# Optimization experiments

Hardware: AMD Instinct MI355X
Metric: run time of the kernel (lower is better)

## Reference

```python
import jax, jax.numpy as jnp
import numpy as np

N_HEADS = 16
D_EMBED = 1024
HEAD_DIM = D_EMBED // N_HEADS


def setup_inputs() -> dict:
    key = jax.random.key(0)
    ks = jax.random.split(key, 9)
    s = 1.0 / np.sqrt(D_EMBED)
    def lin(kw, kb):
        W = jax.random.uniform(kw, (D_EMBED, D_EMBED), jnp.float32, -s, s)
        b = jax.random.uniform(kb, (D_EMBED,), jnp.float32, -s, s)
        return W, b
    q_w, q_b = lin(ks[0], ks[1])
    k_w, k_b = lin(ks[2], ks[3])
    v_w, v_b = lin(ks[4], ks[5])
    o_w, o_b = lin(ks[6], ks[7])
    x = jax.random.normal(ks[8], (4, 2048, D_EMBED), jnp.float32)
    return {"x": x, "q_w": q_w, "q_b": q_b, "k_w": k_w, "k_b": k_b,
            "v_w": v_w, "v_b": v_b, "o_w": o_w, "o_b": o_b}


def reference(x, q_w, q_b, k_w, k_b, v_w, v_b, o_w, o_b):
    B, S, _ = x.shape
    # projections; W stored as [in, out] so y = x @ W + b (matches nn.Linear math)
    def split_heads(y):
        return y.reshape(B, S, N_HEADS, HEAD_DIM).transpose(0, 2, 1, 3)  # [B,H,S,D]
    q = split_heads(x @ q_w + q_b)
    k = split_heads(x @ k_w + k_b)
    v = split_heads(x @ v_w + v_b)
    scale = 1.0 / np.sqrt(HEAD_DIM).astype(np.float32)
    scores = jnp.einsum('bhqd,bhkd->bhqk', q, k) * scale  # [B,H,S,S]
    weights = jax.nn.softmax(scores, axis=-1)
    attn = jnp.einsum('bhqk,bhkd->bhqd', weights, v)  # [B,H,S,D]
    attn = attn.transpose(0, 2, 1, 3).reshape(B, S, D_EMBED)
    return attn @ o_w + o_b
```

## Files before the change

kernel.cpp:

```cpp
#include <hip/hip_runtime.h>
#include <hip/hip_bf16.h>
#include <math.h>

typedef __attribute__((ext_vector_type(8))) short bf16x8;
typedef __attribute__((ext_vector_type(4))) float f32x4;

#define D_EMBED 1024
#define SEQ 2048
#define NH 16
#define HD 64
#define QSCALE 0.1803368801111204f

__device__ __forceinline__ short f2bf(float f) {
    union { float f; unsigned u; } v; v.f = f;
    return (short)((v.u + 0x7FFFu + ((v.u >> 16) & 1u)) >> 16);
}

__device__ __forceinline__ unsigned pk_bf16(float a, float b) {
#if __has_builtin(__builtin_amdgcn_cvt_pk_bf16_f32)
    typedef __attribute__((ext_vector_type(2))) __bf16 vbf2;
    union { vbf2 v; unsigned u; } c;
    c.v = __builtin_amdgcn_cvt_pk_bf16_f32(a, b);
    return c.u;
#else
    return (unsigned)(unsigned short)f2bf(a) | ((unsigned)(unsigned short)f2bf(b) << 16);
#endif
}

__device__ __forceinline__ float exp2f_(float x) {
#if __has_builtin(__builtin_amdgcn_exp2f)
    return __builtin_amdgcn_exp2f(x);
#else
    return __expf(x * 0.6931471805599453f);
#endif
}

typedef __attribute__((address_space(1))) const void gvoid_t;
typedef __attribute__((address_space(3))) void lvoid_t;
__device__ __forceinline__ void glds16(const void* g, void* l) {
    __builtin_amdgcn_global_load_lds((gvoid_t*)g, (lvoid_t*)l, 16, 0, 0);
}

__global__ __launch_bounds__(256) void prep_kernel(
    const float* __restrict__ x,
    const float* __restrict__ w0, const float* __restrict__ w1,
    const float* __restrict__ w2, const float* __restrict__ w3,
    short* __restrict__ wt, short* __restrict__ xb)
{
    __shared__ float tile[64][65];
    const int bid = blockIdx.x;
    if (bid < 1024) {
        const int z = bid >> 8, rem = bid & 255;
        const float* W = (z == 0) ? w0 : (z == 1) ? w1 : (z == 2) ? w2 : w3;
        short* out = wt + (size_t)z * D_EMBED * D_EMBED;
        int k0 = (rem & 15) * 64, n0 = (rem >> 4) * 64;
        #pragma unroll
        for (int i = 0; i < 16; i++) {
            int idx = threadIdx.x + i * 256; int r = idx >> 6, c = idx & 63;
            tile[r][c] = W[(size_t)(k0 + r) * D_EMBED + n0 + c];
        }
        __syncthreads();
        #pragma unroll
        for (int i = 0; i < 16; i++) {
            int idx = threadIdx.x + i * 256; int r = idx >> 6, c = idx & 63;
            out[(size_t)(n0 + r) * D_EMBED + k0 + c] = f2bf(tile[c][r]);
        }
    } else {
        size_t i = ((size_t)(bid - 1024) * 256 + threadIdx.x) * 8;
        float4 f0 = *(const float4*)(x + i);
        float4 f1 = *(const float4*)(x + i + 4);
        uint4 o;
        o.x = pk_bf16(f0.x, f0.y); o.y = pk_bf16(f0.z, f0.w);
        o.z = pk_bf16(f1.x, f1.y); o.w = pk_bf16(f1.z, f1.w);
        *(uint4*)(xb + i) = o;
    }
}

__global__ __launch_bounds__(256) void gemm_qkv_kernel(
    const short* __restrict__ xb, const short* __restrict__ wt,
    const float* __restrict__ qb, const float* __restrict__ kb, const float* __restrict__ vb,
    short* __restrict__ qo, short* __restrict__ ko, short* __restrict__ vto)
{
    __shared__ __attribute__((aligned(16))) union ShQKV {
        struct { short As[128][32]; short Bs[128][32]; } ab;
        short Es[64][136];
    } sh;
    const int tid = threadIdx.x;
    const int lane = tid & 63, wv = tid >> 6;
    const int l16 = lane & 15, quad = lane >> 4;
    const int wm = (wv & 1) * 64, wn = (wv >> 1) * 64;
    const int m0 = blockIdx.y * 128, n0 = blockIdx.x * 128;

    const short* aptr0 = xb + (size_t)(m0 + (tid >> 2)) * D_EMBED + (tid & 3) * 8;
    const short* aptr1 = aptr0 + (size_t)64 * D_EMBED;
    const short* bptr0 = wt + (size_t)(n0 + (tid >> 2)) * D_EMBED + (tid & 3) * 8;
    const short* bptr1 = bptr0 + (size_t)64 * D_EMBED;
    char* aldsb = (char*)&sh.ab.As[0][0] + wv * 1024;
    char* bldsb = (char*)&sh.ab.Bs[0][0] + wv * 1024;

    f32x4 acc[4][4];
    #pragma unroll
    for (int a = 0; a < 4; a++)
        #pragma unroll
        for (int b = 0; b < 4; b++) acc[a][b] = (f32x4){0.f, 0.f, 0.f, 0.f};

    for (int k0 = 0; k0 < D_EMBED; k0 += 32) {
        __syncthreads();
        glds16(aptr0 + k0, aldsb);
        glds16(aptr1 + k0, aldsb + 4096);
        glds16(bptr0 + k0, bldsb);
        glds16(bptr1 + k0, bldsb + 4096);
        __syncthreads();
        bf16x8 af[4], bfr[4];
        #pragma unroll
        for (int mi = 0; mi < 4; mi++) af[mi]  = *(const bf16x8*)&sh.ab.As[wm + mi * 16 + l16][quad * 8];
        #pragma unroll
        for (int ni = 0; ni < 4; ni++) bfr[ni] = *(const bf16x8*)&sh.ab.Bs[wn + ni * 16 + l16][quad * 8];
        #pragma unroll
        for (int mi = 0; mi < 4; mi++)
            #pragma unroll
            for (int ni = 0; ni < 4; ni++)
                acc[mi][ni] = __builtin_amdgcn_mfma_f32_16x16x32_bf16(af[mi], bfr[ni], acc[mi][ni], 0, 0, 0);
    }

    const int zz = n0 >> 10;
    if (zz == 2) {
        const int b = m0 >> 11, st0 = m0 & 2047;
        const int hbase = (n0 & 1023) >> 6;
        #pragma unroll
        for (int h2 = 0; h2 < 2; h2++) {
            __syncthreads();
            if ((wv >> 1) == h2) {
                #pragma unroll
                for (int mi = 0; mi < 4; mi++) {
                    int sbase = (wv & 1) * 64 + mi * 16 + quad * 4;
                    #pragma unroll
                    for (int ni = 0; ni < 4; ni++) {
                        int d = ni * 16 + l16;
                        float bv = vb[(n0 & 1023) + h2 * 64 + d];
                        uint2 pw;
                        pw.x = pk_bf16(acc[mi][ni][0] + bv, acc[mi][ni][1] + bv);
                        pw.y = pk_bf16(acc[mi][ni][2] + bv, acc[mi][ni][3] + bv);
                        *(uint2*)&sh.Es[d][sbase] = pw;
                    }
                }
            }
            __syncthreads();
            const int h = hbase + h2;
            #pragma unroll
            for (int j = 0; j < 4; j++) {
                int d = j * 16 + (tid >> 4);
                int sc = (tid & 15) * 8;
                bf16x8 vv = *(const bf16x8*)&sh.Es[d][sc];
                *(bf16x8*)(vto + ((size_t)(b * NH + h) * HD + d) * SEQ + st0 + sc) = vv;
            }
        }
    } else {
        const int ncol0 = (n0 & 1023) + wn;
        const float* bias = (zz == 0) ? qb : kb;
        #pragma unroll
        for (int mi = 0; mi < 4; mi++)
            #pragma unroll
            for (int ni = 0; ni < 4; ni++)
                #pragma unroll
                for (int rg = 0; rg < 4; rg++) {
                    int row = m0 + wm + mi * 16 + quad * 4 + rg;
                    int col = ncol0 + ni * 16 + l16;
                    float v = acc[mi][ni][rg] + bias[col];
                    int b = row >> 11, s = row & 2047, h = col >> 6, d = col & 63;
                    if (zz == 0) qo[(((size_t)(b * NH + h)) * SEQ + s) * HD + d] = f2bf(v * QSCALE);
                    else         ko[(((size_t)(b * NH + h)) * SEQ + s) * HD + d] = f2bf(v);
                }
    }
}

__global__ __launch_bounds__(256) void flash_kernel(
    const short* __restrict__ Q, const short* __restrict__ K,
    const short* __restrict__ Vt, short* __restrict__ attn)
{
    __shared__ __attribute__((aligned(16))) short Vs[64][64];
    __shared__ __attribute__((aligned(16))) short Ps[4][64][72];
    const int bh = blockIdx.y, qt = blockIdx.x;
    const int tid = threadIdx.x, lane = tid & 63, wv = tid >> 6;
    const int l16 = lane & 15, quad = lane >> 4;
    const int sw = l16 & 7;

    bf16x8 qf[4][2];
    #pragma unroll
    for (int g = 0; g < 4; g++) {
        const short* qp = Q + ((size_t)bh * SEQ + qt * 256 + wv * 64 + g * 16 + l16) * HD;
        qf[g][0] = *(const bf16x8*)(qp + quad * 8);
        qf[g][1] = *(const bf16x8*)(qp + 32 + quad * 8);
    }

    const int sr = tid >> 3;
    const int scg = (tid & 7) ^ (sr & 7);
    const short* vp0 = Vt + ((size_t)bh * HD + sr) * SEQ + scg * 8;
    char* vldsb = (char*)&Vs[0][0] + wv * 1024;

    const short* kb0 = K + ((size_t)bh * SEQ + l16) * HD + quad * 8;

    float lsum[4] = {0.f, 0.f, 0.f, 0.f};
    f32x4 oacc[4][4];
    #pragma unroll
    for (int g = 0; g < 4; g++)
        #pragma unroll
        for (int di = 0; di < 4; di++) oacc[g][di] = (f32x4){0.f, 0.f, 0.f, 0.f};

    for (int kt = 0; kt < SEQ; kt += 64) {
        __syncthreads();
        glds16(vp0 + kt, vldsb);
        glds16(vp0 + (size_t)32 * SEQ + kt, vldsb + 4096);

        bf16x8 kf[4][2];
        #pragma unroll
        for (int ni = 0; ni < 4; ni++) {
            const short* kp = kb0 + (size_t)(kt + ni * 16) * HD;
            kf[ni][0] = *(const bf16x8*)kp;
            kf[ni][1] = *(const bf16x8*)(kp + 32);
        }

        #pragma unroll
        for (int g = 0; g < 4; g++) {
            f32x4 sacc[4];
            #pragma unroll
            for (int ni = 0; ni < 4; ni++) {
                sacc[ni] = (f32x4){0.f, 0.f, 0.f, 0.f};
                sacc[ni] = __builtin_amdgcn_mfma_f32_16x16x32_bf16(kf[ni][0], qf[g][0], sacc[ni], 0, 0, 0);
                sacc[ni] = __builtin_amdgcn_mfma_f32_16x16x32_bf16(kf[ni][1], qf[g][1], sacc[ni], 0, 0, 0);
            }
            short* prow = &Ps[wv][g * 16 + l16][0];
            float ps = 0.f;
            #pragma unroll
            for (int ni = 0; ni < 4; ni++) {
                float p0 = exp2f_(sacc[ni][0]);
                float p1 = exp2f_(sacc[ni][1]);
                float p2 = exp2f_(sacc[ni][2]);
                float p3 = exp2f_(sacc[ni][3]);
                ps += (p0 + p1) + (p2 + p3);
                uint2 pw; pw.x = pk_bf16(p0, p1); pw.y = pk_bf16(p2, p3);
                *(uint2*)(prow + ni * 16 + quad * 4) = pw;
            }
            lsum[g] += ps;
        }

        __syncthreads();

        bf16x8 vf[4][2];
        #pragma unroll
        for (int di = 0; di < 4; di++) {
            vf[di][0] = *(const bf16x8*)&Vs[di * 16 + l16][((quad    ) ^ sw) * 8];
            vf[di][1] = *(const bf16x8*)&Vs[di * 16 + l16][((quad + 4) ^ sw) * 8];
        }
        #pragma unroll
        for (int g = 0; g < 4; g++) {
            const short* prow = &Ps[wv][g * 16 + l16][0];
            bf16x8 pf0 = *(const bf16x8*)(prow + quad * 8);
            bf16x8 pf1 = *(const bf16x8*)(prow + 32 + quad * 8);
            #pragma unroll
            for (int di = 0; di < 4; di++) {
                oacc[g][di] = __builtin_amdgcn_mfma_f32_16x16x32_bf16(pf0, vf[di][0], oacc[g][di], 0, 0, 0);
                oacc[g][di] = __builtin_amdgcn_mfma_f32_16x16x32_bf16(pf1, vf[di][1], oacc[g][di], 0, 0, 0);
            }
        }
    }

    const int b = bh >> 4, h = bh & 15;
    #pragma unroll
    for (int g = 0; g < 4; g++) {
        float l = lsum[g];
        l += __shfl_xor(l, 16);
        l += __shfl_xor(l, 32);
        float rl[4];
        #pragma unroll
        for (int rg = 0; rg < 4; rg++) rl[rg] = 1.0f / __shfl(l, quad * 4 + rg);
        #pragma unroll
        for (int di = 0; di < 4; di++)
            #pragma unroll
            for (int rg = 0; rg < 4; rg++) {
                int s = qt * 256 + wv * 64 + g * 16 + quad * 4 + rg;
                int col = h * HD + di * 16 + l16;
                attn[((size_t)b * SEQ + s) * D_EMBED + col] = f2bf(oacc[g][di][rg] * rl[rg]);
            }
    }
}

__global__ __launch_bounds__(256) void gemm_out_kernel(
    const short* __restrict__ attn, const short* __restrict__ wt_o,
    const float* __restrict__ ob, float* __restrict__ out)
{
    __shared__ __attribute__((aligned(16))) short As[128][32];
    __shared__ __attribute__((aligned(16))) short Bs[64][32];
    const int tid = threadIdx.x;
    const int lane = tid & 63, wv = tid >> 6;
    const int l16 = lane & 15, quad = lane >> 4;
    const int wm = (wv & 1) * 64, wn = (wv >> 1) * 32;
    const int m0 = blockIdx.y * 128, n0 = blockIdx.x * 64;

    const short* aptr0 = attn + (size_t)(m0 + (tid >> 2)) * D_EMBED + (tid & 3) * 8;
    const short* aptr1 = aptr0 + (size_t)64 * D_EMBED;
    const short* bptr0 = wt_o + (size_t)(n0 + (tid >> 2)) * D_EMBED + (tid & 3) * 8;
    char* aldsb = (char*)&As[0][0] + wv * 1024;
    char* bldsb = (char*)&Bs[0][0] + wv * 1024;

    f32x4 acc[4][2];
    #pragma unroll
    for (int a = 0; a < 4; a++)
        #pragma unroll
        for (int b = 0; b < 2; b++) acc[a][b] = (f32x4){0.f, 0.f, 0.f, 0.f};

    for (int k0 = 0; k0 < D_EMBED; k0 += 32) {
        __syncthreads();
        glds16(aptr0 + k0, aldsb);
        glds16(aptr1 + k0, aldsb + 4096);
        glds16(bptr0 + k0, bldsb);
        __syncthreads();
        bf16x8 af[4], bfr[2];
        #pragma unroll
        for (int mi = 0; mi < 4; mi++) af[mi]  = *(const bf16x8*)&As[wm + mi * 16 + l16][quad * 8];
        #pragma unroll
        for (int ni = 0; ni < 2; ni++) bfr[ni] = *(const bf16x8*)&Bs[wn + ni * 16 + l16][quad * 8];
        #pragma unroll
        for (int mi = 0; mi < 4; mi++)
            #pragma unroll
            for (int ni = 0; ni < 2; ni++)
                acc[mi][ni] = __builtin_amdgcn_mfma_f32_16x16x32_bf16(af[mi], bfr[ni], acc[mi][ni], 0, 0, 0);
    }

    #pragma unroll
    for (int mi = 0; mi < 4; mi++)
        #pragma unroll
        for (int ni = 0; ni < 2; ni++)
            #pragma unroll
            for (int rg = 0; rg < 4; rg++) {
                int row = m0 + wm + mi * 16 + quad * 4 + rg;
                int col = n0 + wn + ni * 16 + l16;
                out[(size_t)row * D_EMBED + col] = acc[mi][ni][rg] + ob[col];
            }
}

extern "C" void kernel_launch(void* const* d_in, const int* in_sizes, int n_in,
                              void* d_out, int out_size, void* d_ws, size_t ws_size,
                              hipStream_t stream) {
    const float* x  = (const float*)d_in[0];
    const float* qw = (const float*)d_in[1];
    const float* qb = (const float*)d_in[2];
    const float* kw = (const float*)d_in[3];
    const float* kb = (const float*)d_in[4];
    const float* vw = (const float*)d_in[5];
    const float* vb = (const float*)d_in[6];
    const float* ow = (const float*)d_in[7];
    const float* ob = (const float*)d_in[8];

    char* ws = (char*)d_ws;
    short* xb  = (short*)(ws);
    short* wt  = (short*)(ws + (size_t)(16 << 20));
    short* q   = (short*)(ws + (size_t)(24 << 20));
    short* k   = (short*)(ws + (size_t)(40 << 20));
    short* vt  = (short*)(ws + (size_t)(56 << 20));
    short* at  = xb;

    prep_kernel<<<5120, 256, 0, stream>>>(x, qw, kw, vw, ow, wt, xb);
    gemm_qkv_kernel<<<dim3(24, 64), 256, 0, stream>>>(xb, wt, qb, kb, vb, q, k, vt);
    flash_kernel<<<dim3(8, 64), 256, 0, stream>>>(q, k, vt, at);
    gemm_out_kernel<<<dim3(16, 64), 256, 0, stream>>>(at, wt + (size_t)3 * D_EMBED * D_EMBED, ob, (float*)d_out);
}
```

Baseline: 319.0 us.

## Double-buffer K/V tiles in flash kernel and widen GEMM K-step to 64

After: 346.0 us. 1.08x slower.

```diff
diff --git a/kernel.cpp b/kernel.cpp
--- a/kernel.cpp
+++ b/kernel.cpp
@@ -82,7 +82,7 @@
     short* __restrict__ qo, short* __restrict__ ko, short* __restrict__ vto)
 {
     __shared__ __attribute__((aligned(16))) union ShQKV {
-        struct { short As[128][32]; short Bs[128][32]; } ab;
+        struct { short As[2][128][32]; short Bs[2][128][32]; } ab;
         short Es[64][136];
     } sh;
     const int tid = threadIdx.x;
@@ -95,8 +95,8 @@
     const short* aptr1 = aptr0 + (size_t)64 * D_EMBED;
     const short* bptr0 = wt + (size_t)(n0 + (tid >> 2)) * D_EMBED + (tid & 3) * 8;
     const short* bptr1 = bptr0 + (size_t)64 * D_EMBED;
-    char* aldsb = (char*)&sh.ab.As[0][0] + wv * 1024;
-    char* bldsb = (char*)&sh.ab.Bs[0][0] + wv * 1024;
+    char* aldsb = (char*)&sh.ab.As[0][0][0] + wv * 1024;
+    char* bldsb = (char*)&sh.ab.Bs[0][0][0] + wv * 1024;
 
     f32x4 acc[4][4];
     #pragma unroll
@@ -104,23 +104,30 @@
         #pragma unroll
         for (int b = 0; b < 4; b++) acc[a][b] = (f32x4){0.f, 0.f, 0.f, 0.f};
 
-    for (int k0 = 0; k0 < D_EMBED; k0 += 32) {
+    for (int k0 = 0; k0 < D_EMBED; k0 += 64) {
         __syncthreads();
         glds16(aptr0 + k0, aldsb);
         glds16(aptr1 + k0, aldsb + 4096);
+        glds16(aptr0 + k0 + 32, aldsb + 8192);
+        glds16(aptr1 + k0 + 32, aldsb + 8192 + 4096);
         glds16(bptr0 + k0, bldsb);
         glds16(bptr1 + k0, bldsb + 4096);
-        __syncthreads();
-        bf16x8 af[4], bfr[4];
-        #pragma unroll
-        for (int mi = 0; mi < 4; mi++) af[mi]  = *(const bf16x8*)&sh.ab.As[wm + mi * 16 + l16][quad * 8];
-        #pragma unroll
-        for (int ni = 0; ni < 4; ni++) bfr[ni] = *(const bf16x8*)&sh.ab.Bs[wn + ni * 16 + l16][quad * 8];
-        #pragma unroll
-        for (int mi = 0; mi < 4; mi++)
-            #pragma unroll
-            for (int ni = 0; ni < 4; ni++)
-                acc[mi][ni] = __builtin_amdgcn_mfma_f32_16x16x32_bf16(af[mi], bfr[ni], acc[mi][ni], 0, 0, 0);
+        glds16(bptr0 + k0 + 32, bldsb + 8192);
+        glds16(bptr1 + k0 + 32, bldsb + 8192 + 4096);
+        __syncthreads();
+        #pragma unroll
+        for (int hb = 0; hb < 2; hb++) {
+            bf16x8 af[4], bfr[4];
+            #pragma unroll
+            for (int mi = 0; mi < 4; mi++) af[mi]  = *(const bf16x8*)&sh.ab.As[hb][wm + mi * 16 + l16][quad * 8];
+            #pragma unroll
+            for (int ni = 0; ni < 4; ni++) bfr[ni] = *(const bf16x8*)&sh.ab.Bs[hb][wn + ni * 16 + l16][quad * 8];
+            #pragma unroll
+            for (int mi = 0; mi < 4; mi++)
+                #pragma unroll
+                for (int ni = 0; ni < 4; ni++)
+                    acc[mi][ni] = __builtin_amdgcn_mfma_f32_16x16x32_bf16(af[mi], bfr[ni], acc[mi][ni], 0, 0, 0);
+        }
     }
 
     const int zz = n0 >> 10;
@@ -178,7 +185,8 @@
     const short* __restrict__ Q, const short* __restrict__ K,
     const short* __restrict__ Vt, short* __restrict__ attn)
 {
-    __shared__ __attribute__((aligned(16))) short Vs[64][64];
+    __shared__ __attribute__((aligned(16))) short Ks[2][64][64];
+    __shared__ __attribute__((aligned(16))) short Vs[2][64][64];
     __shared__ __attribute__((aligned(16))) short Ps[4][64][72];
     const int bh = blockIdx.y, qt = blockIdx.x;
     const int tid = threadIdx.x, lane = tid & 63, wv = tid >> 6;
@@ -195,10 +203,10 @@
 
     const int sr = tid >> 3;
     const int scg = (tid & 7) ^ (sr & 7);
+    const short* kp0 = K  + ((size_t)bh * SEQ + sr) * HD + scg * 8;
     const short* vp0 = Vt + ((size_t)bh * HD + sr) * SEQ + scg * 8;
-    char* vldsb = (char*)&Vs[0][0] + wv * 1024;
-
-    const short* kb0 = K + ((size_t)bh * SEQ + l16) * HD + quad * 8;
+    char* kldsb = (char*)&Ks[0][0][0] + wv * 1024;
+    char* vldsb = (char*)&Vs[0][0][0] + wv * 1024;
 
     float lsum[4] = {0.f, 0.f, 0.f, 0.f};
     f32x4 oacc[4][4];
@@ -207,17 +215,27 @@
         #pragma unroll
         for (int di = 0; di < 4; di++) oacc[g][di] = (f32x4){0.f, 0.f, 0.f, 0.f};
 
+    glds16(kp0, kldsb);
+    glds16(kp0 + (size_t)32 * HD, kldsb + 4096);
+    glds16(vp0, vldsb);
+    glds16(vp0 + (size_t)32 * SEQ, vldsb + 4096);
+    __syncthreads();
+
     for (int kt = 0; kt < SEQ; kt += 64) {
-        __syncthreads();
-        glds16(vp0 + kt, vldsb);
-        glds16(vp0 + (size_t)32 * SEQ + kt, vldsb + 4096);
+        const int cur = (kt >> 6) & 1;
+        if (kt + 64 < SEQ) {
+            const int nxt = cur ^ 1;
+            glds16(kp0 + (size_t)(kt + 64) * HD, kldsb + nxt * 8192);
+            glds16(kp0 + (size_t)(kt + 96) * HD, kldsb + nxt * 8192 + 4096);
+            glds16(vp0 + kt + 64, vldsb + nxt * 8192);
+            glds16(vp0 + (size_t)32 * SEQ + kt + 64, vldsb + nxt * 8192 + 4096);
+        }
 
         bf16x8 kf[4][2];
         #pragma unroll
         for (int ni = 0; ni < 4; ni++) {
-            const short* kp = kb0 + (size_t)(kt + ni * 16) * HD;
-            kf[ni][0] = *(const bf16x8*)kp;
-            kf[ni][1] = *(const bf16x8*)(kp + 32);
+            kf[ni][0] = *(const bf16x8*)&Ks[cur][ni * 16 + l16][((quad    ) ^ sw) * 8];
+            kf[ni][1] = *(const bf16x8*)&Ks[cur][ni * 16 + l16][((quad + 4) ^ sw) * 8];
         }
 
         #pragma unroll
@@ -244,13 +262,11 @@
             lsum[g] += ps;
         }
 
-        __syncthreads();
-
         bf16x8 vf[4][2];
         #pragma unroll
         for (int di = 0; di < 4; di++) {
-            vf[di][0] = *(const bf16x8*)&Vs[di * 16 + l16][((quad    ) ^ sw) * 8];
-            vf[di][1] = *(const bf16x8*)&Vs[di * 16 + l16][((quad + 4) ^ sw) * 8];
+            vf[di][0] = *(const bf16x8*)&Vs[cur][di * 16 + l16][((quad    ) ^ sw) * 8];
+            vf[di][1] = *(const bf16x8*)&Vs[cur][di * 16 + l16][((quad + 4) ^ sw) * 8];
         }
         #pragma unroll
         for (int g = 0; g < 4; g++) {
@@ -263,6 +279,8 @@
                 oacc[g][di] = __builtin_amdgcn_mfma_f32_16x16x32_bf16(pf1, vf[di][1], oacc[g][di], 0, 0, 0);
             }
         }
+
+        __syncthreads();
     }
 
     const int b = bh >> 4, h = bh & 15;
@@ -289,8 +307,8 @@
     const short* __restrict__ attn, const short* __restrict__ wt_o,
     const float* __restrict__ ob, float* __restrict__ out)
 {
-    __shared__ __attribute__((aligned(16))) short As[128][32];
-    __shared__ __attribute__((aligned(16))) short Bs[64][32];
+    __shared__ __attribute__((aligned(16))) short As[2][128][32];
+    __shared__ __attribute__((aligned(16))) short Bs[2][64][32];
     const int tid = threadIdx.x;
     const int lane = tid & 63, wv = tid >> 6;
     const int l16 = lane & 15, quad = lane >> 4;
@@ -300,8 +318,8 @@
     const short* aptr0 = attn + (size_t)(m0 + (tid >> 2)) * D_EMBED + (tid & 3) * 8;
     const short* aptr1 = aptr0 + (size_t)64 * D_EMBED;
     const short* bptr0 = wt_o + (size_t)(n0 + (tid >> 2)) * D_EMBED + (tid & 3) * 8;
-    char* aldsb = (char*)&As[0][0] + wv * 1024;
-    char* bldsb = (char*)&Bs[0][0] + wv * 1024;
+    char* aldsb = (char*)&As[0][0][0] + wv * 1024;
+    char* bldsb = (char*)&Bs[0][0][0] + wv * 1024;
 
     f32x4 acc[4][2];
     #pragma unroll
@@ -309,22 +327,28 @@
         #pragma unroll
         for (int b = 0; b < 2; b++) acc[a][b] = (f32x4){0.f, 0.f, 0.f, 0.f};
 
-    for (int k0 = 0; k0 < D_EMBED; k0 += 32) {
+    for (int k0 = 0; k0 < D_EMBED; k0 += 64) {
         __syncthreads();
         glds16(aptr0 + k0, aldsb);
         glds16(aptr1 + k0, aldsb + 4096);
+        glds16(aptr0 + k0 + 32, aldsb + 8192);
+        glds16(aptr1 + k0 + 32, aldsb + 8192 + 4096);
         glds16(bptr0 + k0, bldsb);
-        __syncthreads();
-        bf16x8 af[4], bfr[2];
-        #pragma unroll
-        for (int mi = 0; mi < 4; mi++) af[mi]  = *(const bf16x8*)&As[wm + mi * 16 + l16][quad * 8];
-        #pragma unroll
-        for (int ni = 0; ni < 2; ni++) bfr[ni] = *(const bf16x8*)&Bs[wn + ni * 16 + l16][quad * 8];
-        #pragma unroll
-        for (int mi = 0; mi < 4; mi++)
-            #pragma unroll
-            for (int ni = 0; ni < 2; ni++)
-                acc[mi][ni] = __builtin_amdgcn_mfma_f32_16x16x32_bf16(af[mi], bfr[ni], acc[mi][ni], 0, 0, 0);
+        glds16(bptr0 + k0 + 32, bldsb + 4096);
+        __syncthreads();
+        #pragma unroll
+        for (int hb = 0; hb < 2; hb++) {
+            bf16x8 af[4], bfr[2];
+            #pragma unroll
+            for (int mi = 0; mi < 4; mi++) af[mi]  = *(const bf16x8*)&As[hb][wm + mi * 16 + l16][quad * 8];
+            #pragma unroll
+            for (int ni = 0; ni < 2; ni++) bfr[ni] = *(const bf16x8*)&Bs[hb][wn + ni * 16 + l16][quad * 8];
+            #pragma unroll
+            for (int mi = 0; mi < 4; mi++)
+                #pragma unroll
+                for (int ni = 0; ni < 2; ni++)
+                    acc[mi][ni] = __builtin_amdgcn_mfma_f32_16x16x32_bf16(af[mi], bfr[ni], acc[mi][ni], 0, 0, 0);
+        }
     }
 
     #pragma unroll
```
